# Kernel optimization log

Hardware: AMD Instinct MI355X
Metric: run time of the kernel (lower is better)

The kernel has to match this reference:

```python
import jax, jax.numpy as jnp
import numpy as np

N = 50000      # nodes
E = 800000     # edges (before self-loops)
F = 128        # num_features
H = 64         # hidden_channels
B = 512        # batch_size (num graphs)
NC = 10        # num_classes


def setup_inputs() -> dict:
    key = jax.random.key(0)
    ks = jax.random.split(key, 24)
    rn = lambda k, shp, s=0.05: jax.random.normal(k, shp, jnp.float32) * s
    inp = {}
    inp["x"] = jax.random.normal(ks[0], (N, F), jnp.float32)
    inp["edge_index"] = jax.random.randint(ks[1], (2, E), 0, N)
    inp["batch"] = jnp.sort(jax.random.randint(ks[2], (N,), 0, B))
    # GATConv1: in F -> 4 heads x H (concat)
    inp["W1"] = rn(ks[3], (F, 4 * H)); inp["a_src1"] = rn(ks[4], (4, H))
    inp["a_dst1"] = rn(ks[5], (4, H)); inp["b1"] = rn(ks[6], (4 * H,))
    # GATConv2: in 4H -> 1 head x 2H
    inp["W2"] = rn(ks[7], (4 * H, 2 * H)); inp["a_src2"] = rn(ks[8], (1, 2 * H))
    inp["a_dst2"] = rn(ks[9], (1, 2 * H)); inp["b2"] = rn(ks[10], (2 * H,))
    # GCNConv: in 2H -> H
    inp["Wg"] = rn(ks[11], (2 * H, H)); inp["bg"] = rn(ks[12], (H,))
    # BatchNorms (eval mode: running_mean=0, running_var=1)
    inp["bn1_g"] = 1.0 + rn(ks[13], (4 * H,)); inp["bn1_b"] = rn(ks[14], (4 * H,))
    inp["bn2_g"] = 1.0 + rn(ks[15], (2 * H,)); inp["bn2_b"] = rn(ks[16], (2 * H,))
    inp["bn3_g"] = 1.0 + rn(ks[17], (2 * H,)); inp["bn3_b"] = rn(ks[18], (2 * H,))
    inp["lin1_W"] = rn(ks[19], (H, 128)); inp["lin1_b"] = rn(ks[20], (128,))
    inp["lin2_W"] = rn(ks[21], (128, NC)); inp["lin2_b"] = rn(ks[22], (NC,))
    inp["batch_size"] = B
    return inp


def _gat(x, src, dst, W, a_s, a_d, b, n):
    """PyG GATConv (eval): project, edge attention (leaky_relu 0.2), dst-softmax, scatter."""
    heads, ch = a_s.shape
    h = (x @ W).reshape(n, heads, ch)                       # [N, heads, ch]
    sc_s = (h * a_s).sum(-1)                                # [N, heads]
    sc_d = (h * a_d).sum(-1)
    e = jax.nn.leaky_relu(sc_s[src] + sc_d[dst], 0.2)       # [E2, heads]
    m = jax.ops.segment_max(e, dst, num_segments=n)
    ee = jnp.exp(e - m[dst])
    s = jax.ops.segment_sum(ee, dst, num_segments=n)
    alpha = ee / (s[dst] + 1e-16)                           # edge softmax per dst
    out = jax.ops.segment_sum(h[src] * alpha[:, :, None], dst, num_segments=n)
    return out.reshape(n, heads * ch) + b


def _bn_eval(x, g, b, eps=1e-5):
    # BatchNorm1d eval with running_mean=0, running_var=1
    return x * (g / jnp.sqrt(1.0 + eps)) + b


def reference(x, edge_index, batch, W1, a_src1, a_dst1, b1, W2, a_src2, a_dst2, b2,
              Wg, bg, bn1_g, bn1_b, bn2_g, bn2_b, bn3_g, bn3_b,
              lin1_W, lin1_b, lin2_W, lin2_b, batch_size):
    n = x.shape[0]
    loop = jnp.arange(n)
    src = jnp.concatenate([edge_index[0], loop])            # add self-loops (PyG default)
    dst = jnp.concatenate([edge_index[1], loop])
    lrelu = lambda v: jax.nn.leaky_relu(v, 0.01)            # module's LeakyReLU()

    x1 = _bn_eval(lrelu(_gat(x, src, dst, W1, a_src1, a_dst1, b1, n)), bn1_g, bn1_b)
    x2 = _bn_eval(lrelu(_gat(x1, src, dst, W2, a_src2, a_dst2, b2, n)), bn2_g, bn2_b)

    # GCNConv with symmetric normalization over A + I
    deg = jax.ops.segment_sum(jnp.ones_like(dst, jnp.float32), dst, num_segments=n)
    dis = jnp.where(deg > 0, jax.lax.rsqrt(deg), 0.0)
    h = x2 @ Wg                                             # [N, H]
    msg = h[src] * (dis[src] * dis[dst])[:, None]
    x3 = lrelu(jax.ops.segment_sum(msg, dst, num_segments=n) + bg)

    # global_mean_pool over graphs (dropout is identity in eval)
    sums = jax.ops.segment_sum(x3, batch, num_segments=batch_size)
    cnt = jax.ops.segment_sum(jnp.ones((n,), jnp.float32), batch, num_segments=batch_size)
    pooled = sums / jnp.clip(cnt, 1.0)[:, None]             # [B, H]

    y = lrelu(_bn_eval(pooled @ lin1_W + lin1_b, bn3_g, bn3_b))
    return y @ lin2_W + lin2_b                              # [B, NC]
```

## Files before the change

kernel.cpp:

```cpp
#include <hip/hip_runtime.h>
#include <hip/hip_bf16.h>

#define NN  50000
#define EE  800000
#define NE2 850000
#define NB  512
#define NRT 3125
#define NSB 196

#define BN_RS 0.9999950000374997f

typedef __attribute__((ext_vector_type(8))) short short8;
typedef __attribute__((ext_vector_type(4))) float f32x4;

__device__ __forceinline__ float bf2f(__hip_bfloat16 v) { return __bfloat162float(v); }
__device__ __forceinline__ unsigned short f2b(float v) {
    __hip_bfloat16 b = __float2bfloat16(v);
    return *reinterpret_cast<unsigned short*>(&b);
}
__device__ __forceinline__ float u2f(unsigned short u) {
    union { unsigned u; float f; } c; c.u = ((unsigned)u) << 16; return c.f;
}
__device__ __forceinline__ float4 u42f4(ushort4 v) {
    float4 r; r.x = u2f(v.x); r.y = u2f(v.y); r.z = u2f(v.z); r.w = u2f(v.w); return r;
}
__device__ __forceinline__ float lrelu01(float v) { return v > 0.f ? v : 0.01f * v; }
__device__ __forceinline__ float lrelu02(float v) { return v > 0.f ? v : 0.2f * v; }

__device__ __forceinline__ void edge_sd(const int* __restrict__ ei, int e, int& s, int& d) {
    if (e < EE) { s = ei[e]; d = ei[EE + e]; }
    else        { s = e - EE; d = e - EE; }
}

__device__ __forceinline__ float ldf(const void* p, int i, bool bf) {
    return bf ? bf2f(((const __hip_bfloat16*)p)[i]) : ((const float*)p)[i];
}

#define NSEG 20
#define WTOT 85578
#define XQUADS (NN * 32)
#define PREP_TOT (NN + XQUADS + WTOT + 32768 + 32768 + 8192)
struct SegArgs { const void* src[NSEG]; int off[NSEG]; };

__global__ __launch_bounds__(256) void prep_k(SegArgs a,
                                              const void* __restrict__ x_raw,
                                              ushort4* __restrict__ xb4,
                                              const void* __restrict__ W1r,
                                              const void* __restrict__ W2r,
                                              const void* __restrict__ Wgr,
                                              float* __restrict__ wf,
                                              unsigned short* __restrict__ W1t,
                                              unsigned short* __restrict__ W2t,
                                              unsigned short* __restrict__ Wgt,
                                              int* __restrict__ degi,
                                              int* __restrict__ flag) {
    __shared__ int cnt;
    int t = threadIdx.x;
    if (t == 0) cnt = 0;
    __syncthreads();
    {
        int c = 0;
        const unsigned* xw = (const unsigned*)x_raw;
#pragma unroll
        for (int k = 0; k < 4; ++k) {
            unsigned w = xw[t * 4 + k];
            unsigned ef = (w >> 7) & 0xFFu;
            if (ef >= 100u && ef <= 140u) c++;
        }
        atomicAdd(&cnt, c);
    }
    __syncthreads();
    bool bf = (cnt > 512);
    if (blockIdx.x == 0 && t == 0) *flag = bf ? 1 : 0;

    int i = blockIdx.x * 256 + t;
    if (i >= PREP_TOT) return;
    if (i < NN) { degi[i] = 0; return; }
    i -= NN;
    if (i < XQUADS) {
        ushort4 o;
        if (bf) o = ((const ushort4*)x_raw)[i];
        else {
            float4 v = ((const float4*)x_raw)[i];
            o.x = f2b(v.x); o.y = f2b(v.y); o.z = f2b(v.z); o.w = f2b(v.w);
        }
        xb4[i] = o;
        return;
    }
    i -= XQUADS;
    if (i < WTOT) {
        int s = 0;
#pragma unroll
        for (int k = 1; k < NSEG; ++k) if (i >= a.off[k]) s = k;
        wf[i] = ldf(a.src[s], i - a.off[s], bf);
        return;
    }
    i -= WTOT;
    if (i < 32768) {
        int n = i >> 7, k = i & 127;
        W1t[i] = f2b(ldf(W1r, k * 256 + n, bf));
        return;
    }
    i -= 32768;
    if (i < 32768) {
        int n = i >> 8, k = i & 255;
        W2t[i] = f2b(ldf(W2r, k * 128 + n, bf));
        return;
    }
    i -= 32768;
    {
        int n = i >> 7, k = i & 127;
        Wgt[i] = f2b(ldf(Wgr, k * 64 + n, bf));
    }
}

__global__ __launch_bounds__(256) void deg_k(const int* __restrict__ ei, int* __restrict__ degi) {
    int e = blockIdx.x * 256 + threadIdx.x;
    if (e >= NE2) return;
    int s, d; edge_sd(ei, e, s, d);
    atomicAdd(&degi[d], 1);
}

__global__ __launch_bounds__(256) void pscan_k(const int* __restrict__ degi,
                                               int* __restrict__ incl, int* __restrict__ bsum) {
    __shared__ int tmp[256];
    int t = threadIdx.x;
    int i = blockIdx.x * 256 + t;
    int v = (i < NN) ? degi[i] : 0;
    tmp[t] = v;
    __syncthreads();
#pragma unroll
    for (int off = 1; off < 256; off <<= 1) {
        int u = (t >= off) ? tmp[t - off] : 0;
        __syncthreads();
        tmp[t] += u;
        __syncthreads();
    }
    if (i < NN) incl[i] = tmp[t];
    if (t == 255) bsum[blockIdx.x] = tmp[255];
}

__global__ __launch_bounds__(256) void bscan_k(int* __restrict__ bsum) {
    __shared__ int tmp[256];
    int t = threadIdx.x;
    tmp[t] = (t < NSB) ? bsum[t] : 0;
    __syncthreads();
#pragma unroll
    for (int off = 1; off < 256; off <<= 1) {
        int u = (t >= off) ? tmp[t - off] : 0;
        __syncthreads();
        tmp[t] += u;
        __syncthreads();
    }
    if (t < NSB) bsum[t] = tmp[t];
}

__global__ __launch_bounds__(256) void fscan_k(const int* __restrict__ degi,
                                               const int* __restrict__ incl,
                                               const int* __restrict__ bsum,
                                               const int* __restrict__ batch,
                                               int* __restrict__ row_ptr, int* __restrict__ cursor,
                                               float* __restrict__ dis, int* __restrict__ gstart) {
    int i = blockIdx.x * 256 + threadIdx.x;
    if (i <= NB) {
        int lo = 0, hi = NN;
        while (lo < hi) { int mid = (lo + hi) >> 1; if (batch[mid] < i) lo = mid + 1; else hi = mid; }
        gstart[i] = lo;
    }
    if (i >= NN) return;
    int dg = degi[i];
    int base = (blockIdx.x > 0) ? bsum[blockIdx.x - 1] : 0;
    int ex = base + incl[i] - dg;
    row_ptr[i] = ex; cursor[i] = ex;
    dis[i] = dg > 0 ? rsqrtf((float)dg) : 0.f;
    if (i == NN - 1) row_ptr[NN] = bsum[NSB - 1];
}

__global__ __launch_bounds__(256) void scatter_k(const int* __restrict__ ei,
                                                 int* __restrict__ cursor,
                                                 int* __restrict__ csr_src) {
    int e = blockIdx.x * 256 + threadIdx.x;
    if (e >= NE2) return;
    int s, d; edge_sd(ei, e, s, d);
    int pos = atomicAdd(&cursor[d], 1);
    csr_src[pos] = s;
}

__global__ __launch_bounds__(256) void mgemm1_k(const short* __restrict__ A,
                                                const short* __restrict__ Bt,
                                                unsigned short* __restrict__ C,
                                                const float* __restrict__ a_s,
                                                const float* __restrict__ a_d,
                                                float* __restrict__ sc_s,
                                                float* __restrict__ sc_d) {
    int wave = threadIdx.x >> 6, lane = threadIdx.x & 63;
    int rt = blockIdx.x, cg = wave;
    int l15 = lane & 15, quad = lane >> 4;
    const short* ap = A + (size_t)(rt * 16 + l15) * 128 + quad * 8;
    const short* bp = Bt + (size_t)(cg * 64 + l15) * 128 + quad * 8;
    f32x4 acc[4] = {};
    for (int k0 = 0; k0 < 128; k0 += 32) {
        short8 a = *(const short8*)(ap + k0);
#pragma unroll
        for (int j = 0; j < 4; ++j) {
            short8 b = *(const short8*)(bp + (size_t)j * 16 * 128 + k0);
            acc[j] = __builtin_amdgcn_mfma_f32_16x16x32_bf16(a, b, acc[j], 0, 0, 0);
        }
    }
    float asv[4], adv[4];
#pragma unroll
    for (int j = 0; j < 4; ++j) {
        asv[j] = a_s[cg * 64 + j * 16 + l15];
        adv[j] = a_d[cg * 64 + j * 16 + l15];
    }
    float ss[4] = {0.f, 0.f, 0.f, 0.f}, sd[4] = {0.f, 0.f, 0.f, 0.f};
#pragma unroll
    for (int j = 0; j < 4; ++j) {
        int n = cg * 64 + j * 16 + l15;
#pragma unroll
        for (int r = 0; r < 4; ++r) {
            float v = acc[j][r];
            C[(size_t)(rt * 16 + quad * 4 + r) * 256 + n] = f2b(v);
            ss[r] = fmaf(v, asv[j], ss[r]);
            sd[r] = fmaf(v, adv[j], sd[r]);
        }
    }
#pragma unroll
    for (int off = 1; off < 16; off <<= 1) {
#pragma unroll
        for (int r = 0; r < 4; ++r) {
            ss[r] += __shfl_xor(ss[r], off);
            sd[r] += __shfl_xor(sd[r], off);
        }
    }
    if (l15 == 0) {
#pragma unroll
        for (int r = 0; r < 4; ++r) {
            int node = rt * 16 + quad * 4 + r;
            sc_s[node * 4 + cg] = ss[r];
            sc_d[node * 4 + cg] = sd[r];
        }
    }
}

__global__ __launch_bounds__(256) void mgemm2_k(const short* __restrict__ A,
                                                const short* __restrict__ Bt,
                                                unsigned short* __restrict__ C,
                                                const float* __restrict__ a_s,
                                                const float* __restrict__ a_d,
                                                float* __restrict__ sc_s,
                                                float* __restrict__ sc_d) {
    __shared__ float sred[4][16][2];
    int wave = threadIdx.x >> 6, lane = threadIdx.x & 63;
    int gidx = blockIdx.x * 4 + wave;
    bool act = gidx < NRT * 2;
    int gcl = act ? gidx : NRT * 2 - 1;
    int rt = gcl >> 1, cg = gcl & 1;
    int l15 = lane & 15, quad = lane >> 4;
    const short* ap = A + (size_t)(rt * 16 + l15) * 256 + quad * 8;
    const short* bp = Bt + (size_t)(cg * 64 + l15) * 256 + quad * 8;
    f32x4 acc[4] = {};
    for (int k0 = 0; k0 < 256; k0 += 32) {
        short8 a = *(const short8*)(ap + k0);
#pragma unroll
        for (int j = 0; j < 4; ++j) {
            short8 b = *(const short8*)(bp + (size_t)j * 16 * 256 + k0);
            acc[j] = __builtin_amdgcn_mfma_f32_16x16x32_bf16(a, b, acc[j], 0, 0, 0);
        }
    }
    float asv[4], adv[4];
#pragma unroll
    for (int j = 0; j < 4; ++j) {
        asv[j] = a_s[cg * 64 + j * 16 + l15];
        adv[j] = a_d[cg * 64 + j * 16 + l15];
    }
    float ss[4] = {0.f, 0.f, 0.f, 0.f}, sd[4] = {0.f, 0.f, 0.f, 0.f};
#pragma unroll
    for (int j = 0; j < 4; ++j) {
        int n = cg * 64 + j * 16 + l15;
#pragma unroll
        for (int r = 0; r < 4; ++r) {
            float v = acc[j][r];
            if (act) C[(size_t)(rt * 16 + quad * 4 + r) * 128 + n] = f2b(v);
            ss[r] = fmaf(v, asv[j], ss[r]);
            sd[r] = fmaf(v, adv[j], sd[r]);
        }
    }
#pragma unroll
    for (int off = 1; off < 16; off <<= 1) {
#pragma unroll
        for (int r = 0; r < 4; ++r) {
            ss[r] += __shfl_xor(ss[r], off);
            sd[r] += __shfl_xor(sd[r], off);
        }
    }
    if (l15 == 0) {
#pragma unroll
        for (int r = 0; r < 4; ++r) {
            sred[wave][quad * 4 + r][0] = ss[r];
            sred[wave][quad * 4 + r][1] = sd[r];
        }
    }
    __syncthreads();
    if (threadIdx.x < 32) {
        int rl = threadIdx.x >> 4, row = threadIdx.x & 15;
        int g2 = blockIdx.x * 4 + rl * 2;
        if (g2 < NRT * 2) {
            int node = (g2 >> 1) * 16 + row;
            sc_s[node] = sred[rl * 2][row][0] + sred[rl * 2 + 1][row][0];
            sc_d[node] = sred[rl * 2][row][1] + sred[rl * 2 + 1][row][1];
        }
    }
}

__global__ __launch_bounds__(256) void mgemm3_k(const short* __restrict__ A,
                                                const short* __restrict__ Bt,
                                                unsigned short* __restrict__ C) {
    int wave = threadIdx.x >> 6, lane = threadIdx.x & 63;
    int gidx = blockIdx.x * 4 + wave;
    if (gidx >= NRT) return;
    int rt = gidx;
    int l15 = lane & 15, quad = lane >> 4;
    const short* ap = A + (size_t)(rt * 16 + l15) * 128 + quad * 8;
    const short* bp = Bt + (size_t)l15 * 128 + quad * 8;
    f32x4 acc[4] = {};
    for (int k0 = 0; k0 < 128; k0 += 32) {
        short8 a = *(const short8*)(ap + k0);
#pragma unroll
        for (int j = 0; j < 4; ++j) {
            short8 b = *(const short8*)(bp + (size_t)j * 16 * 128 + k0);
            acc[j] = __builtin_amdgcn_mfma_f32_16x16x32_bf16(a, b, acc[j], 0, 0, 0);
        }
    }
#pragma unroll
    for (int j = 0; j < 4; ++j) {
        int n = j * 16 + l15;
#pragma unroll
        for (int r = 0; r < 4; ++r)
            C[(size_t)(rt * 16 + quad * 4 + r) * 64 + n] = f2b(acc[j][r]);
    }
}

__device__ __forceinline__ float sel4(float4 v, int head) {
    float ab = (head & 1) ? v.y : v.x;
    float cd = (head & 1) ? v.w : v.z;
    return (head & 2) ? cd : ab;
}

__global__ __launch_bounds__(256) void agg1_k(const int* __restrict__ row_ptr,
                                              const int* __restrict__ csr_src,
                                              const ushort4* __restrict__ h1b,
                                              const float4* __restrict__ sc_s4,
                                              const float4* __restrict__ sc_d4,
                                              const float4* __restrict__ b1,
                                              const float4* __restrict__ g1,
                                              const float4* __restrict__ bb1,
                                              ushort4* __restrict__ x1b) {
    int n = __builtin_amdgcn_readfirstlane((blockIdx.x * 256 + threadIdx.x) >> 6);
    int lane = threadIdx.x & 63;
    if (n >= NN) return;
    int row = row_ptr[n], end = row_ptr[n + 1];
    int head = lane >> 4;
    float scd_h = sel4(sc_d4[n], head);
    float4 acc = {0.f, 0.f, 0.f, 0.f};
    float den = 0.f;
    int c = row;
    for (; c + 7 < end; c += 8) {
        int s[8];
#pragma unroll
        for (int j = 0; j < 8; ++j) s[j] = csr_src[c + j];
        float4 scs[8];
#pragma unroll
        for (int j = 0; j < 8; ++j) scs[j] = sc_s4[s[j]];
        ushort4 hu[8];
#pragma unroll
        for (int j = 0; j < 8; ++j) hu[j] = h1b[(size_t)s[j] * 64 + lane];
        float e[8];
#pragma unroll
        for (int j = 0; j < 8; ++j) { e[j] = __expf(lrelu02(sel4(scs[j], head) + scd_h)); den += e[j]; }
#pragma unroll
        for (int j = 0; j < 8; ++j) {
            float4 hv = u42f4(hu[j]);
            acc.x = fmaf(hv.x, e[j], acc.x);
            acc.y = fmaf(hv.y, e[j], acc.y);
            acc.z = fmaf(hv.z, e[j], acc.z);
            acc.w = fmaf(hv.w, e[j], acc.w);
        }
    }
    for (; c + 3 < end; c += 4) {
        int s[4];
#pragma unroll
        for (int j = 0; j < 4; ++j) s[j] = csr_src[c + j];
        float4 scs[4];
#pragma unroll
        for (int j = 0; j < 4; ++j) scs[j] = sc_s4[s[j]];
        ushort4 hu[4];
#pragma unroll
        for (int j = 0; j < 4; ++j) hu[j] = h1b[(size_t)s[j] * 64 + lane];
#pragma unroll
        for (int j = 0; j < 4; ++j) {
            float e0 = __expf(lrelu02(sel4(scs[j], head) + scd_h));
            den += e0;
            float4 hv = u42f4(hu[j]);
            acc.x = fmaf(hv.x, e0, acc.x);
            acc.y = fmaf(hv.y, e0, acc.y);
            acc.z = fmaf(hv.z, e0, acc.z);
            acc.w = fmaf(hv.w, e0, acc.w);
        }
    }
    for (; c < end; ++c) {
        int s0 = csr_src[c];
        float4 scs0 = sc_s4[s0];
        float4 hv0 = u42f4(h1b[(size_t)s0 * 64 + lane]);
        float e0 = __expf(lrelu02(sel4(scs0, head) + scd_h));
        den += e0;
        acc.x = fmaf(hv0.x, e0, acc.x);
        acc.y = fmaf(hv0.y, e0, acc.y);
        acc.z = fmaf(hv0.z, e0, acc.z);
        acc.w = fmaf(hv0.w, e0, acc.w);
    }
    float inv = 1.f / (den + 1e-16f);
    float4 bb = b1[lane], gg = g1[lane], be = bb1[lane];
    ushort4 o;
    o.x = f2b(lrelu01(acc.x * inv + bb.x) * (gg.x * BN_RS) + be.x);
    o.y = f2b(lrelu01(acc.y * inv + bb.y) * (gg.y * BN_RS) + be.y);
    o.z = f2b(lrelu01(acc.z * inv + bb.z) * (gg.z * BN_RS) + be.z);
    o.w = f2b(lrelu01(acc.w * inv + bb.w) * (gg.w * BN_RS) + be.w);
    x1b[(size_t)n * 64 + lane] = o;
}

__global__ __launch_bounds__(256) void agg2_k(const int* __restrict__ row_ptr,
                                              const int* __restrict__ csr_src,
                                              const ushort4* __restrict__ h2b,
                                              const float* __restrict__ sc_s,
                                              const float* __restrict__ sc_d,
                                              const float4* __restrict__ b2,
                                              const float4* __restrict__ g2,
                                              const float4* __restrict__ bb2,
                                              ushort4* __restrict__ x2b) {
    int n = __builtin_amdgcn_readfirstlane((blockIdx.x * 256 + threadIdx.x) >> 6);
    int lane = threadIdx.x & 63;
    if (n >= NN) return;
    int g = lane >> 5, sl = lane & 31;
    int row = row_ptr[n], end = row_ptr[n + 1];
    float scd = sc_d[n];
    float4 acc = {0.f, 0.f, 0.f, 0.f};
    float den = 0.f;
    int c = row + g;
    for (; c + 6 < end; c += 8) {
        int s[4];
#pragma unroll
        for (int j = 0; j < 4; ++j) s[j] = csr_src[c + 2 * j];
        float sc[4];
#pragma unroll
        for (int j = 0; j < 4; ++j) sc[j] = sc_s[s[j]];
        ushort4 hu[4];
#pragma unroll
        for (int j = 0; j < 4; ++j) hu[j] = h2b[(size_t)s[j] * 32 + sl];
#pragma unroll
        for (int j = 0; j < 4; ++j) {
            float e0 = __expf(lrelu02(sc[j] + scd));
            den += e0;
            float4 hv = u42f4(hu[j]);
            acc.x = fmaf(hv.x, e0, acc.x);
            acc.y = fmaf(hv.y, e0, acc.y);
            acc.z = fmaf(hv.z, e0, acc.z);
            acc.w = fmaf(hv.w, e0, acc.w);
        }
    }
    for (; c < end; c += 2) {
        int s0 = csr_src[c];
        float e0 = __expf(lrelu02(sc_s[s0] + scd));
        float4 hv0 = u42f4(h2b[(size_t)s0 * 32 + sl]);
        den += e0;
        acc.x = fmaf(hv0.x, e0, acc.x);
        acc.y = fmaf(hv0.y, e0, acc.y);
        acc.z = fmaf(hv0.z, e0, acc.z);
        acc.w = fmaf(hv0.w, e0, acc.w);
    }
    den += __shfl_xor(den, 32);
    acc.x += __shfl_xor(acc.x, 32);
    acc.y += __shfl_xor(acc.y, 32);
    acc.z += __shfl_xor(acc.z, 32);
    acc.w += __shfl_xor(acc.w, 32);
    if (g == 0) {
        float inv = 1.f / (den + 1e-16f);
        float4 bb = b2[sl], gg = g2[sl], be = bb2[sl];
        ushort4 o;
        o.x = f2b(lrelu01(acc.x * inv + bb.x) * (gg.x * BN_RS) + be.x);
        o.y = f2b(lrelu01(acc.y * inv + bb.y) * (gg.y * BN_RS) + be.y);
        o.z = f2b(lrelu01(acc.z * inv + bb.z) * (gg.z * BN_RS) + be.z);
        o.w = f2b(lrelu01(acc.w * inv + bb.w) * (gg.w * BN_RS) + be.w);
        x2b[(size_t)n * 32 + sl] = o;
    }
}

__global__ __launch_bounds__(256) void gcn_k(const int* __restrict__ row_ptr,
                                             const int* __restrict__ csr_src,
                                             const ushort4* __restrict__ hgb,
                                             const float* __restrict__ dis,
                                             const float4* __restrict__ bg,
                                             float4* __restrict__ x3) {
    int n = __builtin_amdgcn_readfirstlane((blockIdx.x * 256 + threadIdx.x) >> 6);
    int lane = threadIdx.x & 63;
    if (n >= NN) return;
    int g = lane >> 4, sl = lane & 15;
    int row = row_ptr[n], end = row_ptr[n + 1];
    float dn = dis[n];
    float4 acc = {0.f, 0.f, 0.f, 0.f};
    int c = row + g;
    for (; c + 12 < end; c += 16) {
        int s[4];
#pragma unroll
        for (int j = 0; j < 4; ++j) s[j] = csr_src[c + 4 * j];
        float w[4];
#pragma unroll
        for (int j = 0; j < 4; ++j) w[j] = dis[s[j]];
        ushort4 hu[4];
#pragma unroll
        for (int j = 0; j < 4; ++j) hu[j] = hgb[(size_t)s[j] * 16 + sl];
#pragma unroll
        for (int j = 0; j < 4; ++j) {
            float4 hv = u42f4(hu[j]);
            acc.x = fmaf(hv.x, w[j], acc.x);
            acc.y = fmaf(hv.y, w[j], acc.y);
            acc.z = fmaf(hv.z, w[j], acc.z);
            acc.w = fmaf(hv.w, w[j], acc.w);
        }
    }
    for (; c < end; c += 4) {
        int s0 = csr_src[c];
        float w0 = dis[s0];
        float4 hv0 = u42f4(hgb[(size_t)s0 * 16 + sl]);
        acc.x = fmaf(hv0.x, w0, acc.x);
        acc.y = fmaf(hv0.y, w0, acc.y);
        acc.z = fmaf(hv0.z, w0, acc.z);
        acc.w = fmaf(hv0.w, w0, acc.w);
    }
#pragma unroll
    for (int off = 16; off <= 32; off <<= 1) {
        acc.x += __shfl_xor(acc.x, off);
        acc.y += __shfl_xor(acc.y, off);
        acc.z += __shfl_xor(acc.z, off);
        acc.w += __shfl_xor(acc.w, off);
    }
    if (g == 0) {
        float4 bb = bg[sl];
        float4 o;
        o.x = lrelu01(acc.x * dn + bb.x);
        o.y = lrelu01(acc.y * dn + bb.y);
        o.z = lrelu01(acc.z * dn + bb.z);
        o.w = lrelu01(acc.w * dn + bb.w);
        x3[(size_t)n * 16 + sl] = o;
    }
}

__global__ __launch_bounds__(256) void pool_k(const float* __restrict__ x3,
                                              const int* __restrict__ gstart,
                                              float* __restrict__ pooled) {
    __shared__ float red[4][64];
    int g = blockIdx.x, t = threadIdx.x;
    int c = t & 63, r = t >> 6;
    int s = gstart[g], e = gstart[g + 1];
    float sum = 0.f;
    for (int n = s + r; n < e; n += 4) sum += x3[(size_t)n * 64 + c];
    red[r][c] = sum;
    __syncthreads();
    if (t < 64) {
        float v = red[0][t] + red[1][t] + red[2][t] + red[3][t];
        int cnt = e - s; if (cnt < 1) cnt = 1;
        pooled[g * 64 + t] = v / (float)cnt;
    }
}

__global__ __launch_bounds__(128) void mlp_k(const float* __restrict__ pooled,
                                             const float* __restrict__ l1W,
                                             const float* __restrict__ l1b,
                                             const float* __restrict__ g3,
                                             const float* __restrict__ b3,
                                             const float* __restrict__ l2W,
                                             const float* __restrict__ l2b,
                                             void* __restrict__ outp,
                                             const int* __restrict__ flag) {
    __shared__ float pl[64];
    __shared__ float y1s[128];
    int g = blockIdx.x, t = threadIdx.x;
    if (t < 64) pl[t] = pooled[g * 64 + t];
    __syncthreads();
    float acc = l1b[t];
#pragma unroll 8
    for (int j = 0; j < 64; ++j) acc = fmaf(pl[j], l1W[j * 128 + t], acc);
    acc = acc * (g3[t] * BN_RS) + b3[t];
    y1s[t] = lrelu01(acc);
    __syncthreads();
    if (t < 10) {
        float o = l2b[t];
#pragma unroll 8
        for (int j = 0; j < 128; ++j) o = fmaf(y1s[j], l2W[j * 10 + t], o);
        if (*flag) ((__hip_bfloat16*)outp)[g * 10 + t] = __float2bfloat16(o);
        else       ((float*)outp)[g * 10 + t] = o;
    }
}

static const int kSegN[NSEG]  = {32768, 256, 256, 256, 32768, 128, 128, 128, 8192, 64,
                                 256, 256, 128, 128, 128, 128, 8192, 128, 1280, 10};
static const int kSegIn[NSEG] = {3, 4, 5, 6, 7, 8, 9, 10, 11, 12, 13, 14, 15, 16, 17, 18, 19, 20, 21, 22};

extern "C" void kernel_launch(void* const* d_in, const int* in_sizes, int n_in,
                              void* d_out, int out_size, void* d_ws, size_t ws_size,
                              hipStream_t stream) {
    const void* x_raw = d_in[0];
    const int*  ei    = (const int*)d_in[1];
    const int*  batch = (const int*)d_in[2];

    int*   flag = (int*)d_ws;
    float* ws   = (float*)d_ws;
    unsigned short* xb = (unsigned short*)(ws + 16);
    float* wf   = ws + 16 + (size_t)NN * 64;
    unsigned short* W1t = (unsigned short*)(wf + 85584);
    unsigned short* W2t = W1t + 32768;
    unsigned short* Wgt = W2t + 32768;
    unsigned short* h1b = Wgt + 8192;
    unsigned short* x1b = h1b + (size_t)NN * 256;
    unsigned short* x2b = x1b + (size_t)NN * 256;
    unsigned short* hgb = x2b + (size_t)NN * 128;
    float* x3   = (float*)(hgb + (size_t)NN * 64);
    float* sc_s1 = x3 + (size_t)NN * 64;
    float* sc_d1 = sc_s1 + (size_t)NN * 4;
    float* sc_s2 = sc_d1 + (size_t)NN * 4;
    float* sc_d2 = sc_s2 + NN;
    float* disb  = sc_d2 + NN;
    float* pooled = disb + NN;
    int*   gstart = (int*)(pooled + NB * 64);
    int*   degi   = gstart + NB + 4;
    int*   incl   = degi + NN;
    int*   bsum   = incl + NN;
    int*   row_ptr = bsum + 256;
    int*   cursor  = row_ptr + NN + 1;
    int*   csr_src = cursor + NN;

    int off[NSEG]; int o = 0;
    for (int s = 0; s < NSEG; ++s) { off[s] = o; o += kSegN[s]; }
    float* as1f = wf + off[1];  float* ad1f = wf + off[2];
    float* b1f  = wf + off[3];  float* as2f = wf + off[5];
    float* ad2f = wf + off[6];  float* b2f  = wf + off[7];
    float* bgf  = wf + off[9];  float* bn1g = wf + off[10]; float* bn1b = wf + off[11];
    float* bn2g = wf + off[12]; float* bn2b = wf + off[13]; float* bn3g = wf + off[14];
    float* bn3b = wf + off[15]; float* l1Wf = wf + off[16]; float* l1bf = wf + off[17];
    float* l2Wf = wf + off[18]; float* l2bf = wf + off[19];

    unsigned short* h2b = h1b;

    SegArgs sa;
    for (int s = 0; s < NSEG; ++s) { sa.src[s] = d_in[kSegIn[s]]; sa.off[s] = off[s]; }
    prep_k<<<(PREP_TOT + 255) / 256, 256, 0, stream>>>(sa, x_raw, (ushort4*)xb,
                                                       d_in[3], d_in[7], d_in[11],
                                                       wf, W1t, W2t, Wgt, degi, flag);

    deg_k<<<(NE2 + 255) / 256, 256, 0, stream>>>(ei, degi);
    pscan_k<<<NSB, 256, 0, stream>>>(degi, incl, bsum);
    bscan_k<<<1, 256, 0, stream>>>(bsum);
    fscan_k<<<NSB, 256, 0, stream>>>(degi, incl, bsum, batch, row_ptr, cursor, disb, gstart);
    scatter_k<<<(NE2 + 255) / 256, 256, 0, stream>>>(ei, cursor, csr_src);

    mgemm1_k<<<NRT, 256, 0, stream>>>((const short*)xb, (const short*)W1t, h1b,
                                      as1f, ad1f, sc_s1, sc_d1);
    agg1_k<<<12500, 256, 0, stream>>>(row_ptr, csr_src, (const ushort4*)h1b,
                                      (const float4*)sc_s1, (const float4*)sc_d1,
                                      (const float4*)b1f, (const float4*)bn1g,
                                      (const float4*)bn1b, (ushort4*)x1b);

    mgemm2_k<<<(NRT * 2 + 3) / 4, 256, 0, stream>>>((const short*)x1b, (const short*)W2t, h2b,
                                                    as2f, ad2f, sc_s2, sc_d2);
    agg2_k<<<12500, 256, 0, stream>>>(row_ptr, csr_src, (const ushort4*)h2b,
                                      sc_s2, sc_d2,
                                      (const float4*)b2f, (const float4*)bn2g,
                                      (const float4*)bn2b, (ushort4*)x2b);

    mgemm3_k<<<(NRT + 3) / 4, 256, 0, stream>>>((const short*)x2b, (const short*)Wgt, hgb);
    gcn_k<<<12500, 256, 0, stream>>>(row_ptr, csr_src, (const ushort4*)hgb, disb,
                                     (const float4*)bgf, (float4*)x3);
    pool_k<<<NB, 256, 0, stream>>>(x3, gstart, pooled);

    mlp_k<<<NB, 128, 0, stream>>>(pooled, l1Wf, l1bf, bn3g, bn3b, l2Wf, l2bf, d_out, flag);
}
```

Measured before the change: 455.9 us.

## Fuse degree count into prep, fuse pool with MLP, restructure agg2/gcn edge loads

Degree counting moves into the prep kernel, with a memset replacing the in-kernel zeroing, and pooling is fused with the MLP head. Together these remove two kernel launches and the pooled intermediate buffer. agg2 and gcn now load contiguous blocks of CSR indices and attention scores per thread and pick each lane-group's edge with selects, which aims to coalesce index loads and raise memory-level parallelism. agg1 loses its 4-wide remainder loop, and the wider unrolls raise register pressure.

```diff
diff --git a/kernel.cpp b/kernel.cpp
--- a/kernel.cpp
+++ b/kernel.cpp
@@ -39,7 +39,7 @@
 #define NSEG 20
 #define WTOT 85578
 #define XQUADS (NN * 32)
-#define PREP_TOT (NN + XQUADS + WTOT + 32768 + 32768 + 8192)
+#define PREP_TOT (XQUADS + WTOT + 32768 + 32768 + 8192 + NE2)
 struct SegArgs { const void* src[NSEG]; int off[NSEG]; };
 
 __global__ __launch_bounds__(256) void prep_k(SegArgs a,
@@ -52,6 +52,7 @@
                                               unsigned short* __restrict__ W1t,
                                               unsigned short* __restrict__ W2t,
                                               unsigned short* __restrict__ Wgt,
+                                              const int* __restrict__ ei,
                                               int* __restrict__ degi,
                                               int* __restrict__ flag) {
     __shared__ int cnt;
@@ -75,8 +76,6 @@
 
     int i = blockIdx.x * 256 + t;
     if (i >= PREP_TOT) return;
-    if (i < NN) { degi[i] = 0; return; }
-    i -= NN;
     if (i < XQUADS) {
         ushort4 o;
         if (bf) o = ((const ushort4*)x_raw)[i];
@@ -108,17 +107,16 @@
         return;
     }
     i -= 32768;
-    {
+    if (i < 8192) {
         int n = i >> 7, k = i & 127;
         Wgt[i] = f2b(ldf(Wgr, k * 64 + n, bf));
-    }
-}
-
-__global__ __launch_bounds__(256) void deg_k(const int* __restrict__ ei, int* __restrict__ degi) {
-    int e = blockIdx.x * 256 + threadIdx.x;
-    if (e >= NE2) return;
-    int s, d; edge_sd(ei, e, s, d);
-    atomicAdd(&degi[d], 1);
+        return;
+    }
+    i -= 8192;
+    {
+        int s, d; edge_sd(ei, i, s, d);
+        atomicAdd(&degi[d], 1);
+    }
 }
 
 __global__ __launch_bounds__(256) void pscan_k(const int* __restrict__ degi,
@@ -387,27 +385,6 @@
             acc.w = fmaf(hv.w, e[j], acc.w);
         }
     }
-    for (; c + 3 < end; c += 4) {
-        int s[4];
-#pragma unroll
-        for (int j = 0; j < 4; ++j) s[j] = csr_src[c + j];
-        float4 scs[4];
-#pragma unroll
-        for (int j = 0; j < 4; ++j) scs[j] = sc_s4[s[j]];
-        ushort4 hu[4];
-#pragma unroll
-        for (int j = 0; j < 4; ++j) hu[j] = h1b[(size_t)s[j] * 64 + lane];
-#pragma unroll
-        for (int j = 0; j < 4; ++j) {
-            float e0 = __expf(lrelu02(sel4(scs[j], head) + scd_h));
-            den += e0;
-            float4 hv = u42f4(hu[j]);
-            acc.x = fmaf(hv.x, e0, acc.x);
-            acc.y = fmaf(hv.y, e0, acc.y);
-            acc.z = fmaf(hv.z, e0, acc.z);
-            acc.w = fmaf(hv.w, e0, acc.w);
-        }
-    }
     for (; c < end; ++c) {
         int s0 = csr_src[c];
         float4 scs0 = sc_s4[s0];
@@ -446,37 +423,41 @@
     float scd = sc_d[n];
     float4 acc = {0.f, 0.f, 0.f, 0.f};
     float den = 0.f;
-    int c = row + g;
-    for (; c + 6 < end; c += 8) {
-        int s[4];
-#pragma unroll
-        for (int j = 0; j < 4; ++j) s[j] = csr_src[c + 2 * j];
-        float sc[4];
-#pragma unroll
-        for (int j = 0; j < 4; ++j) sc[j] = sc_s[s[j]];
+    int c = row;
+    for (; c + 7 < end; c += 8) {
+        int s[8];
+#pragma unroll
+        for (int j = 0; j < 8; ++j) s[j] = csr_src[c + j];
+        float sc[8];
+#pragma unroll
+        for (int j = 0; j < 8; ++j) sc[j] = sc_s[s[j]];
         ushort4 hu[4];
 #pragma unroll
-        for (int j = 0; j < 4; ++j) hu[j] = h2b[(size_t)s[j] * 32 + sl];
-#pragma unroll
-        for (int j = 0; j < 4; ++j) {
-            float e0 = __expf(lrelu02(sc[j] + scd));
-            den += e0;
-            float4 hv = u42f4(hu[j]);
-            acc.x = fmaf(hv.x, e0, acc.x);
-            acc.y = fmaf(hv.y, e0, acc.y);
-            acc.z = fmaf(hv.z, e0, acc.z);
-            acc.w = fmaf(hv.w, e0, acc.w);
-        }
-    }
-    for (; c < end; c += 2) {
-        int s0 = csr_src[c];
-        float e0 = __expf(lrelu02(sc_s[s0] + scd));
-        float4 hv0 = u42f4(h2b[(size_t)s0 * 32 + sl]);
-        den += e0;
-        acc.x = fmaf(hv0.x, e0, acc.x);
-        acc.y = fmaf(hv0.y, e0, acc.y);
-        acc.z = fmaf(hv0.z, e0, acc.z);
-        acc.w = fmaf(hv0.w, e0, acc.w);
+        for (int k = 0; k < 4; ++k) {
+            int sg = g ? s[2 * k + 1] : s[2 * k];
+            hu[k] = h2b[(size_t)sg * 32 + sl];
+        }
+#pragma unroll
+        for (int k = 0; k < 4; ++k) {
+            float scg = g ? sc[2 * k + 1] : sc[2 * k];
+            float e = __expf(lrelu02(scg + scd));
+            den += e;
+            float4 hv = u42f4(hu[k]);
+            acc.x = fmaf(hv.x, e, acc.x);
+            acc.y = fmaf(hv.y, e, acc.y);
+            acc.z = fmaf(hv.z, e, acc.z);
+            acc.w = fmaf(hv.w, e, acc.w);
+        }
+    }
+    for (int cc = c + g; cc < end; cc += 2) {
+        int s0 = csr_src[cc];
+        float e = __expf(lrelu02(sc_s[s0] + scd));
+        den += e;
+        float4 hv = u42f4(h2b[(size_t)s0 * 32 + sl]);
+        acc.x = fmaf(hv.x, e, acc.x);
+        acc.y = fmaf(hv.y, e, acc.y);
+        acc.z = fmaf(hv.z, e, acc.z);
+        acc.w = fmaf(hv.w, e, acc.w);
     }
     den += __shfl_xor(den, 32);
     acc.x += __shfl_xor(acc.x, 32);
@@ -508,28 +489,36 @@
     int row = row_ptr[n], end = row_ptr[n + 1];
     float dn = dis[n];
     float4 acc = {0.f, 0.f, 0.f, 0.f};
-    int c = row + g;
-    for (; c + 12 < end; c += 16) {
-        int s[4];
-#pragma unroll
-        for (int j = 0; j < 4; ++j) s[j] = csr_src[c + 4 * j];
-        float w[4];
-#pragma unroll
-        for (int j = 0; j < 4; ++j) w[j] = dis[s[j]];
+    int c = row;
+    for (; c + 15 < end; c += 16) {
+        int s[16];
+#pragma unroll
+        for (int j = 0; j < 16; ++j) s[j] = csr_src[c + j];
+        float w[16];
+#pragma unroll
+        for (int j = 0; j < 16; ++j) w[j] = dis[s[j]];
         ushort4 hu[4];
 #pragma unroll
-        for (int j = 0; j < 4; ++j) hu[j] = hgb[(size_t)s[j] * 16 + sl];
-#pragma unroll
-        for (int j = 0; j < 4; ++j) {
-            float4 hv = u42f4(hu[j]);
-            acc.x = fmaf(hv.x, w[j], acc.x);
-            acc.y = fmaf(hv.y, w[j], acc.y);
-            acc.z = fmaf(hv.z, w[j], acc.z);
-            acc.w = fmaf(hv.w, w[j], acc.w);
-        }
-    }
-    for (; c < end; c += 4) {
-        int s0 = csr_src[c];
+        for (int k = 0; k < 4; ++k) {
+            int sg0 = (g & 1) ? s[4 * k + 1] : s[4 * k];
+            int sg1 = (g & 1) ? s[4 * k + 3] : s[4 * k + 2];
+            int sg = (g & 2) ? sg1 : sg0;
+            hu[k] = hgb[(size_t)sg * 16 + sl];
+        }
+#pragma unroll
+        for (int k = 0; k < 4; ++k) {
+            float w0 = (g & 1) ? w[4 * k + 1] : w[4 * k];
+            float w1 = (g & 1) ? w[4 * k + 3] : w[4 * k + 2];
+            float wg = (g & 2) ? w1 : w0;
+            float4 hv = u42f4(hu[k]);
+            acc.x = fmaf(hv.x, wg, acc.x);
+            acc.y = fmaf(hv.y, wg, acc.y);
+            acc.z = fmaf(hv.z, wg, acc.z);
+            acc.w = fmaf(hv.w, wg, acc.w);
+        }
+    }
+    for (int cc = c + g; cc < end; cc += 4) {
+        int s0 = csr_src[cc];
         float w0 = dis[s0];
         float4 hv0 = u42f4(hgb[(size_t)s0 * 16 + sl]);
         acc.x = fmaf(hv0.x, w0, acc.x);
@@ -555,10 +544,19 @@
     }
 }
 
-__global__ __launch_bounds__(256) void pool_k(const float* __restrict__ x3,
-                                              const int* __restrict__ gstart,
-                                              float* __restrict__ pooled) {
+__global__ __launch_bounds__(256) void poolmlp_k(const float* __restrict__ x3,
+                                                 const int* __restrict__ gstart,
+                                                 const float* __restrict__ l1W,
+                                                 const float* __restrict__ l1b,
+                                                 const float* __restrict__ g3,
+                                                 const float* __restrict__ b3,
+                                                 const float* __restrict__ l2W,
+                                                 const float* __restrict__ l2b,
+                                                 void* __restrict__ outp,
+                                                 const int* __restrict__ flag) {
     __shared__ float red[4][64];
+    __shared__ float pl[64];
+    __shared__ float y1s[128];
     int g = blockIdx.x, t = threadIdx.x;
     int c = t & 63, r = t >> 6;
     int s = gstart[g], e = gstart[g + 1];
@@ -569,29 +567,16 @@
     if (t < 64) {
         float v = red[0][t] + red[1][t] + red[2][t] + red[3][t];
         int cnt = e - s; if (cnt < 1) cnt = 1;
-        pooled[g * 64 + t] = v / (float)cnt;
-    }
-}
-
-__global__ __launch_bounds__(128) void mlp_k(const float* __restrict__ pooled,
-                                             const float* __restrict__ l1W,
-                                             const float* __restrict__ l1b,
-                                             const float* __restrict__ g3,
-                                             const float* __restrict__ b3,
-                                             const float* __restrict__ l2W,
-                                             const float* __restrict__ l2b,
-                                             void* __restrict__ outp,
-                                             const int* __restrict__ flag) {
-    __shared__ float pl[64];
-    __shared__ float y1s[128];
-    int g = blockIdx.x, t = threadIdx.x;
-    if (t < 64) pl[t] = pooled[g * 64 + t];
-    __syncthreads();
-    float acc = l1b[t];
+        pl[t] = v / (float)cnt;
+    }
+    __syncthreads();
+    if (t < 128) {
+        float acc = l1b[t];
 #pragma unroll 8
-    for (int j = 0; j < 64; ++j) acc = fmaf(pl[j], l1W[j * 128 + t], acc);
-    acc = acc * (g3[t] * BN_RS) + b3[t];
-    y1s[t] = lrelu01(acc);
+        for (int j = 0; j < 64; ++j) acc = fmaf(pl[j], l1W[j * 128 + t], acc);
+        acc = acc * (g3[t] * BN_RS) + b3[t];
+        y1s[t] = lrelu01(acc);
+    }
     __syncthreads();
     if (t < 10) {
         float o = l2b[t];
@@ -630,8 +615,7 @@
     float* sc_s2 = sc_d1 + (size_t)NN * 4;
     float* sc_d2 = sc_s2 + NN;
     float* disb  = sc_d2 + NN;
-    float* pooled = disb + NN;
-    int*   gstart = (int*)(pooled + NB * 64);
+    int*   gstart = (int*)(disb + NN);
     int*   degi   = gstart + NB + 4;
     int*   incl   = degi + NN;
     int*   bsum   = incl + NN;
@@ -651,13 +635,13 @@
 
     unsigned short* h2b = h1b;
 
+    hipMemsetAsync(degi, 0, NN * sizeof(int), stream);
     SegArgs sa;
     for (int s = 0; s < NSEG; ++s) { sa.src[s] = d_in[kSegIn[s]]; sa.off[s] = off[s]; }
     prep_k<<<(PREP_TOT + 255) / 256, 256, 0, stream>>>(sa, x_raw, (ushort4*)xb,
                                                        d_in[3], d_in[7], d_in[11],
-                                                       wf, W1t, W2t, Wgt, degi, flag);
-
-    deg_k<<<(NE2 + 255) / 256, 256, 0, stream>>>(ei, degi);
+                                                       wf, W1t, W2t, Wgt, ei, degi, flag);
+
     pscan_k<<<NSB, 256, 0, stream>>>(degi, incl, bsum);
     bscan_k<<<1, 256, 0, stream>>>(bsum);
     fscan_k<<<NSB, 256, 0, stream>>>(degi, incl, bsum, batch, row_ptr, cursor, disb, gstart);
@@ -680,7 +664,6 @@
     mgemm3_k<<<(NRT + 3) / 4, 256, 0, stream>>>((const short*)x2b, (const short*)Wgt, hgb);
     gcn_k<<<12500, 256, 0, stream>>>(row_ptr, csr_src, (const ushort4*)hgb, disb,
                                      (const float4*)bgf, (float4*)x3);
-    pool_k<<<NB, 256, 0, stream>>>(x3, gstart, pooled);
-
-    mlp_k<<<NB, 128, 0, stream>>>(pooled, l1Wf, l1bf, bn3g, bn3b, l2Wf, l2bf, d_out, flag);
-}
+    poolmlp_k<<<NB, 256, 0, stream>>>(x3, gstart, l1Wf, l1bf, bn3g, bn3b, l2Wf, l2bf,
+                                      d_out, flag);
+}
```

New measurement: 749.5 us. +64.4%, slower.
